# Optimization experiments

Hardware: AMD Instinct MI355X
Metric: run time of the kernel (lower is better)

## Reference

```python
import jax, jax.numpy as jnp
import numpy as np
import math

B, S, HID, H = 2, 2048, 1024, 16
D = HID // H  # head_dim = 64

def _get_slopes(n):
    # power-of-2 branch (n=16)
    start = 2 ** (-2 ** (-(math.log2(n) - 3)))
    return np.array([start * 2 ** (-i) for i in range(n)], dtype=np.float32)

def setup_inputs() -> dict:
    key = jax.random.key(0)
    ks = jax.random.split(key, 9)
    sc = 1.0 / math.sqrt(HID)
    return {
        "x":  jax.random.normal(ks[0], (B, S, HID), dtype=jnp.float32),
        "Wq": jax.random.normal(ks[1], (HID, HID), dtype=jnp.float32) * sc,
        "bq": jnp.zeros((HID,), dtype=jnp.float32),
        "Wk": jax.random.normal(ks[2], (HID, HID), dtype=jnp.float32) * sc,
        "bk": jnp.zeros((HID,), dtype=jnp.float32),
        "Wv": jax.random.normal(ks[3], (HID, HID), dtype=jnp.float32) * sc,
        "bv": jnp.zeros((HID,), dtype=jnp.float32),
        "Wo": jax.random.normal(ks[4], (HID, HID), dtype=jnp.float32) * sc,
        "bo": jnp.zeros((HID,), dtype=jnp.float32),
        "slopes": jnp.asarray(_get_slopes(H)),
    }

def reference(x, Wq, bq, Wk, bk, Wv, bv, Wo, bo, slopes):
    b, s, hid = x.shape
    h = slopes.shape[0]
    d = hid // h
    # projections (torch Linear: y = x @ W.T + b), split heads -> [b,h,s,d]
    q = (x @ Wq.T + bq).reshape(b, s, h, d).transpose(0, 2, 1, 3)
    k = (x @ Wk.T + bk).reshape(b, s, h, d).transpose(0, 2, 1, 3)
    v = (x @ Wv.T + bv).reshape(b, s, h, d).transpose(0, 2, 1, 3)
    scores = jnp.einsum('bhqd,bhkd->bhqk', q, k) / jnp.sqrt(jnp.float32(d))
    # ALiBi bias: slope_h * (j - i), shape [h,s,s]
    pos = jnp.arange(s)
    dist = (pos[None, :] - pos[:, None]).astype(x.dtype)  # [s,s]
    scores = scores + slopes[None, :, None, None] * dist[None, None]
    attn = jax.nn.softmax(scores, axis=-1)
    ctx = jnp.einsum('bhqk,bhkd->bhqd', attn, v)
    ctx = ctx.transpose(0, 2, 1, 3).reshape(b, s, hid)
    return ctx @ Wo.T + bo
```

## Files before the change

kernel.cpp:

```cpp
#include <hip/hip_runtime.h>
#include <stdint.h>

typedef __attribute__((ext_vector_type(8))) short bf16x8;
typedef __attribute__((ext_vector_type(4))) short bf16x4;
typedef __attribute__((ext_vector_type(4))) float f32x4;
typedef unsigned short u16t;

#define DEVINL static __device__ __forceinline__

DEVINL u16t f2bf(float f) {
  union { float f; unsigned u; } v; v.f = f;
  return (u16t)((v.u + 0x7FFFu + ((v.u >> 16) & 1u)) >> 16);
}

DEVINL float exp2_fast(float x) {
  float r; asm("v_exp_f32 %0, %1" : "=v"(r) : "v"(x)); return r;
}
DEVINL unsigned cvt_pk_bf16(float a, float b) {
  unsigned r; asm("v_cvt_pk_bf16_f32 %0, %1, %2" : "=v"(r) : "v"(a), "v"(b)); return r;
}

DEVINL void gload16(const void* g, void* l) {
  __builtin_amdgcn_global_load_lds((const __attribute__((address_space(1))) void*)g,
                                   (__attribute__((address_space(3))) void*)l, 16, 0, 0);
}

__global__ __launch_bounds__(256)
void cvt5_kernel(const float* __restrict__ x, const float* __restrict__ wq,
                 const float* __restrict__ wk, const float* __restrict__ wv,
                 const float* __restrict__ wo, u16t* __restrict__ x_bf,
                 u16t* __restrict__ wqkv, u16t* __restrict__ wo_bf) {
  const int bid = blockIdx.x;
  const float* src; u16t* dst; int off;
  if (bid < 2048) { src = x; dst = x_bf; off = bid * 2048; }
  else {
    const int j = bid - 2048, sel = j >> 9;
    off = (j & 511) * 2048;
    if (sel == 0)      { src = wq; dst = wqkv; }
    else if (sel == 1) { src = wk; dst = wqkv + 1048576; }
    else if (sel == 2) { src = wv; dst = wqkv + 2097152; }
    else               { src = wo; dst = wo_bf; }
  }
  const int i = off + threadIdx.x * 8;
  float4 a = *(const float4*)(src + i);
  float4 b = *(const float4*)(src + i + 4);
  union { bf16x8 v; u16t u[8]; } o;
  o.u[0] = f2bf(a.x); o.u[1] = f2bf(a.y); o.u[2] = f2bf(a.z); o.u[3] = f2bf(a.w);
  o.u[4] = f2bf(b.x); o.u[5] = f2bf(b.y); o.u[6] = f2bf(b.z); o.u[7] = f2bf(b.w);
  *(bf16x8*)(dst + i) = o.v;
}

template <int MODE>
__global__ __launch_bounds__(256, 2)
void gemm_kernel(const u16t* __restrict__ A, const u16t* __restrict__ Bw,
                 const float* __restrict__ bias0, const float* __restrict__ bias1,
                 const float* __restrict__ bias2, void* __restrict__ outp) {
  __shared__ __attribute__((aligned(16))) u16t As[128 * 64];
  __shared__ __attribute__((aligned(16))) u16t Bs[128 * 64];
  const int tid = threadIdx.x;
  const int w = tid >> 6, l = tid & 63;
  const int wm = w >> 1, wn = w & 1;
  const int bm = blockIdx.x, bn = blockIdx.y;
  const int g = l >> 4, r16 = l & 15;
  const int srow = l >> 3, sslot = l & 7;

  f32x4 acc[4][4];
#pragma unroll
  for (int m = 0; m < 4; ++m)
#pragma unroll
    for (int n = 0; n < 4; ++n) acc[m][n] = f32x4{0.f, 0.f, 0.f, 0.f};

  const size_t arow0 = (size_t)bm * 128;
  const size_t brow0 = (size_t)bn * 128;

  for (int kt = 0; kt < 16; ++kt) {
    __syncthreads();
#pragma unroll
    for (int i = 0; i < 4; ++i) {
      const int row = (i * 4 + w) * 8 + srow;
      const int colA = kt * 64 + ((sslot ^ (row & 7)) * 8);
      gload16(A + (arow0 + row) * 1024 + colA, (char*)As + (i * 4 + w) * 1024);
      gload16(Bw + (brow0 + row) * 1024 + colA, (char*)Bs + (i * 4 + w) * 1024);
    }
    asm volatile("s_waitcnt vmcnt(0)" ::: "memory");
    __syncthreads();
#pragma unroll
    for (int kk = 0; kk < 2; ++kk) {
      bf16x8 af[4], bfr[4];
#pragma unroll
      for (int m = 0; m < 4; ++m) {
        const int rr = wm * 64 + m * 16 + r16;
        af[m] = *(const bf16x8*)((const char*)As + rr * 128 + (((kk * 4 + g) ^ (rr & 7)) * 16));
      }
#pragma unroll
      for (int n = 0; n < 4; ++n) {
        const int rr = wn * 64 + n * 16 + r16;
        bfr[n] = *(const bf16x8*)((const char*)Bs + rr * 128 + (((kk * 4 + g) ^ (rr & 7)) * 16));
      }
#pragma unroll
      for (int m = 0; m < 4; ++m)
#pragma unroll
        for (int n = 0; n < 4; ++n)
          acc[m][n] = __builtin_amdgcn_mfma_f32_16x16x32_bf16(af[m], bfr[n], acc[m][n], 0, 0, 0);
    }
  }

  if (MODE == 0) {
    const int mat = bn >> 3;
    if (mat == 2) {
      u16t* vt = (u16t*)outp + 8388608u;
#pragma unroll
      for (int n = 0; n < 4; ++n) {
        const int col = ((bn & 7) * 128) + wn * 64 + n * 16 + r16;
        const int hh = col >> 6, dd = col & 63;
        const float bv = bias2[col];
#pragma unroll
        for (int m = 0; m < 4; ++m) {
          const int row0 = bm * 128 + wm * 64 + m * 16 + g * 4;
          const int b_ = row0 >> 11, s_ = row0 & 2047;
          union { bf16x4 v; u16t u[4]; } o4;
#pragma unroll
          for (int i = 0; i < 4; ++i) o4.u[i] = f2bf(acc[m][n][i] + bv);
          *(bf16x4*)(vt + ((size_t)(b_ * 16 + hh) * 64 + dd) * 2048 + s_) = o4.v;
        }
      }
    } else {
      const float* bias = (mat == 0) ? bias0 : bias1;
      const float scale = (mat == 0) ? 0.18033688f : 1.0f;
      u16t* o = (u16t*)outp + (size_t)mat * 4194304u;
#pragma unroll
      for (int n = 0; n < 4; ++n) {
        const int col = ((bn & 7) * 128) + wn * 64 + n * 16 + r16;
        const float bv = bias[col];
#pragma unroll
        for (int m = 0; m < 4; ++m) {
          const int row = bm * 128 + wm * 64 + m * 16 + g * 4;
#pragma unroll
          for (int i = 0; i < 4; ++i)
            o[(size_t)(row + i) * 1024 + col] = f2bf((acc[m][n][i] + bv) * scale);
        }
      }
    }
  } else {
    float* o = (float*)outp;
#pragma unroll
    for (int n = 0; n < 4; ++n) {
      const int col = bn * 128 + wn * 64 + n * 16 + r16;
      const float bv = bias0[col];
#pragma unroll
      for (int m = 0; m < 4; ++m) {
        const int row = bm * 128 + wm * 64 + m * 16 + g * 4;
#pragma unroll
        for (int i = 0; i < 4; ++i)
          o[(size_t)(row + i) * 1024 + col] = acc[m][n][i] + bv;
      }
    }
  }
}

__global__ __launch_bounds__(256, 2)
void attn_kernel(const u16t* __restrict__ Qb, const u16t* __restrict__ Kb,
                 const u16t* __restrict__ Vtb, const float* __restrict__ slopes,
                 u16t* __restrict__ Ctx) {
  __shared__ __attribute__((aligned(16))) u16t Kl[2][4096];
  __shared__ __attribute__((aligned(16))) u16t Vl[2][4096];
  const int tid = threadIdx.x;
  const int w = tid >> 6, l = tid & 63;
  const int g = l >> 4, r = l & 15;
  const int qt = blockIdx.x, bh = blockIdx.y;
  const int b = bh >> 4, h = bh & 15;
  const float slope2 = slopes[h] * 1.44269504f;
  const int qpos = qt * 64 + w * 16 + r;
  const size_t base = (size_t)b * 2097152 + (size_t)h * 64;

  const u16t* qrow = Qb + base + (size_t)qpos * 1024;
  const bf16x8 qf0 = *(const bf16x8*)(qrow + g * 8);
  const bf16x8 qf1 = *(const bf16x8*)(qrow + 32 + g * 8);

  const int sig = 8 * (r >> 2) + (r & 3);
  const int toffs[4] = {0, 4, 32, 36};
  int koff[4][2], voff[4][2];
#pragma unroll
  for (int t = 0; t < 4; ++t) {
    const int row = toffs[t] + sig;
    const int mk = (row & 3) ^ ((row >> 1) & 4);
#pragma unroll
    for (int hh = 0; hh < 2; ++hh) koff[t][hh] = row * 128 + (((hh * 4 + g) ^ mk) * 16);
  }
#pragma unroll
  for (int db = 0; db < 4; ++db) {
    const int row = 16 * db + r;
#pragma unroll
    for (int hh = 0; hh < 2; ++hh) voff[db][hh] = row * 128 + (((hh * 4 + g) ^ (row & 7)) * 16);
  }

  int k_row[2], k_u[2], v_u[2];
#pragma unroll
  for (int p = 0; p < 2; ++p) {
    const int line = p * 32 + w * 8 + (l >> 3);
    k_row[p] = line;
    k_u[p] = ((l & 7) ^ ((line & 3) ^ ((line >> 1) & 4))) * 8;
    v_u[p] = ((l & 7) ^ (line & 7)) * 8;
  }

  f32x4 cv[4];
#pragma unroll
  for (int t = 0; t < 4; ++t)
#pragma unroll
    for (int i = 0; i < 4; ++i) cv[t][i] = slope2 * (float)(toffs[t] + 8 * g + i);

  const float d64 = slope2 * 64.f;
  float mj = -3.0e38f;
  f32x4 oc[4], sacc;
#pragma unroll
  for (int d = 0; d < 4; ++d) oc[d] = f32x4{0.f, 0.f, 0.f, 0.f};
  sacc = f32x4{0.f, 0.f, 0.f, 0.f};
  union { bf16x8 v; u16t u[8]; } ones;
#pragma unroll
  for (int i = 0; i < 8; ++i) ones.u[i] = 0x3F80;

  const u16t* Krow = Kb + base;
  const u16t* Vrow = Vtb + (size_t)(b * 16 + h) * 131072;

#pragma unroll
  for (int p = 0; p < 2; ++p) {
    gload16(Krow + (size_t)(31 * 64 + k_row[p]) * 1024 + k_u[p],
            (char*)Kl + p * 4096 + w * 1024);
    gload16(Vrow + (size_t)k_row[p] * 2048 + 31 * 64 + v_u[p],
            (char*)Vl + p * 4096 + w * 1024);
  }

  for (int it = 0; it < 32; ++it) {
    const int kt = 31 - it;
    const int buf = it & 1;
    __syncthreads();
    if (it) mj += d64;
    if (it + 1 < 32) {
      const int nb = buf ^ 1, nkt = kt - 1;
#pragma unroll
      for (int p = 0; p < 2; ++p) {
        gload16(Krow + (size_t)(nkt * 64 + k_row[p]) * 1024 + k_u[p],
                (char*)Kl + nb * 8192 + p * 4096 + w * 1024);
        gload16(Vrow + (size_t)k_row[p] * 2048 + nkt * 64 + v_u[p],
                (char*)Vl + nb * 8192 + p * 4096 + w * 1024);
      }
    }
    const char* KB = (const char*)Kl + buf * 8192;
    const char* VB = (const char*)Vl + buf * 8192;

    f32x4 st[4];
#pragma unroll
    for (int t = 0; t < 4; ++t) {
      st[t] = __builtin_amdgcn_mfma_f32_16x16x32_bf16(
          *(const bf16x8*)(KB + koff[t][0]), qf0, cv[t], 0, 0, 0);
      st[t] = __builtin_amdgcn_mfma_f32_16x16x32_bf16(
          *(const bf16x8*)(KB + koff[t][1]), qf1, st[t], 0, 0, 0);
    }

    float tm = fmaxf(fmaxf(st[0][0], st[0][1]), fmaxf(st[0][2], st[0][3]));
    tm = fmaxf(tm, fmaxf(fmaxf(st[1][0], st[1][1]), fmaxf(st[1][2], st[1][3])));
    tm = fmaxf(tm, fmaxf(fmaxf(st[2][0], st[2][1]), fmaxf(st[2][2], st[2][3])));
    tm = fmaxf(tm, fmaxf(fmaxf(st[3][0], st[3][1]), fmaxf(st[3][2], st[3][3])));
    if (__any(tm > mj)) {
      float tr = fmaxf(tm, __shfl_xor(tm, 16));
      tr = fmaxf(tr, __shfl_xor(tr, 32));
      const float mn = fmaxf(mj, tr);
      const float corr = exp2_fast(mj - mn);
#pragma unroll
      for (int d = 0; d < 4; ++d) {
        oc[d][0] *= corr; oc[d][1] *= corr; oc[d][2] *= corr; oc[d][3] *= corr;
      }
      sacc[0] *= corr; sacc[1] *= corr; sacc[2] *= corr; sacc[3] *= corr;
      mj = mn;
    }

    float pe[16];
#pragma unroll
    for (int t = 0; t < 4; ++t)
#pragma unroll
      for (int i = 0; i < 4; ++i) pe[t * 4 + i] = exp2_fast(st[t][i] - mj);
    union { bf16x8 v; unsigned q[4]; } pb0, pb1;
#pragma unroll
    for (int j = 0; j < 4; ++j) {
      pb0.q[j] = cvt_pk_bf16(pe[j * 2], pe[j * 2 + 1]);
      pb1.q[j] = cvt_pk_bf16(pe[8 + j * 2], pe[8 + j * 2 + 1]);
    }

#pragma unroll
    for (int db = 0; db < 4; ++db) {
      oc[db] = __builtin_amdgcn_mfma_f32_16x16x32_bf16(
          *(const bf16x8*)(VB + voff[db][0]), pb0.v, oc[db], 0, 0, 0);
      oc[db] = __builtin_amdgcn_mfma_f32_16x16x32_bf16(
          *(const bf16x8*)(VB + voff[db][1]), pb1.v, oc[db], 0, 0, 0);
    }
    sacc = __builtin_amdgcn_mfma_f32_16x16x32_bf16(ones.v, pb0.v, sacc, 0, 0, 0);
    sacc = __builtin_amdgcn_mfma_f32_16x16x32_bf16(ones.v, pb1.v, sacc, 0, 0, 0);
  }

  const float inv = 1.0f / sacc[0];
  u16t* orow = Ctx + base + (size_t)qpos * 1024;
#pragma unroll
  for (int d = 0; d < 4; ++d) {
    union { bf16x4 v; u16t u[4]; } o4;
#pragma unroll
    for (int i = 0; i < 4; ++i) o4.u[i] = f2bf(oc[d][i] * inv);
    *(bf16x4*)(orow + d * 16 + g * 4) = o4.v;
  }
}

extern "C" void kernel_launch(void* const* d_in, const int* in_sizes, int n_in,
                              void* d_out, int out_size, void* d_ws, size_t ws_size,
                              hipStream_t stream) {
  const float* x = (const float*)d_in[0];
  const float* Wq = (const float*)d_in[1];
  const float* bq = (const float*)d_in[2];
  const float* Wk = (const float*)d_in[3];
  const float* bk = (const float*)d_in[4];
  const float* Wv = (const float*)d_in[5];
  const float* bv = (const float*)d_in[6];
  const float* Wo = (const float*)d_in[7];
  const float* bo = (const float*)d_in[8];
  const float* slopes = (const float*)d_in[9];
  if (ws_size < (size_t)(48u << 20)) return;
  char* ws = (char*)d_ws;
  u16t* x_bf = (u16t*)(ws);
  u16t* wqkv = (u16t*)(ws + (8u << 20));
  u16t* wo_bf = (u16t*)(ws + (14u << 20));
  u16t* q_bf = (u16t*)(ws + (16u << 20));
  u16t* ctx_bf = (u16t*)(ws + (40u << 20));

  cvt5_kernel<<<4096, 256, 0, stream>>>(x, Wq, Wk, Wv, Wo, x_bf, wqkv, wo_bf);
  gemm_kernel<0><<<dim3(32, 24), 256, 0, stream>>>(x_bf, wqkv, bq, bk, bv, (void*)q_bf);
  attn_kernel<<<dim3(32, 32), 256, 0, stream>>>(q_bf, q_bf + 4194304, q_bf + 8388608,
                                                slopes, ctx_bf);
  gemm_kernel<1><<<dim3(32, 8), 256, 0, stream>>>(ctx_bf, wo_bf, bo, bo, bo, d_out);
}
```

Measured before the change: 121.0 us.

## Triple-buffer K/V tiles with explicit vmcnt waits and use max3 reductions

```diff
diff --git a/kernel.cpp b/kernel.cpp
--- a/kernel.cpp
+++ b/kernel.cpp
@@ -18,6 +18,9 @@
 }
 DEVINL unsigned cvt_pk_bf16(float a, float b) {
   unsigned r; asm("v_cvt_pk_bf16_f32 %0, %1, %2" : "=v"(r) : "v"(a), "v"(b)); return r;
+}
+DEVINL float max3f(float a, float b, float c) {
+  float r; asm("v_max3_f32 %0, %1, %2, %3" : "=v"(r) : "v"(a), "v"(b), "v"(c)); return r;
 }
 
 DEVINL void gload16(const void* g, void* l) {
@@ -162,8 +165,8 @@
 void attn_kernel(const u16t* __restrict__ Qb, const u16t* __restrict__ Kb,
                  const u16t* __restrict__ Vtb, const float* __restrict__ slopes,
                  u16t* __restrict__ Ctx) {
-  __shared__ __attribute__((aligned(16))) u16t Kl[2][4096];
-  __shared__ __attribute__((aligned(16))) u16t Vl[2][4096];
+  __shared__ __attribute__((aligned(16))) u16t Kl[3][4096];
+  __shared__ __attribute__((aligned(16))) u16t Vl[3][4096];
   const int tid = threadIdx.x;
   const int w = tid >> 6, l = tid & 63;
   const int g = l >> 4, r = l & 15;
@@ -176,6 +179,7 @@
   const u16t* qrow = Qb + base + (size_t)qpos * 1024;
   const bf16x8 qf0 = *(const bf16x8*)(qrow + g * 8);
   const bf16x8 qf1 = *(const bf16x8*)(qrow + 32 + g * 8);
+  asm volatile("s_waitcnt vmcnt(0)" ::: "memory");
 
   const int sig = 8 * (r >> 2) + (r & 3);
   const int toffs[4] = {0, 4, 32, 36};
@@ -222,29 +226,30 @@
   const u16t* Krow = Kb + base;
   const u16t* Vrow = Vtb + (size_t)(b * 16 + h) * 131072;
 
-#pragma unroll
-  for (int p = 0; p < 2; ++p) {
-    gload16(Krow + (size_t)(31 * 64 + k_row[p]) * 1024 + k_u[p],
-            (char*)Kl + p * 4096 + w * 1024);
-    gload16(Vrow + (size_t)k_row[p] * 2048 + 31 * 64 + v_u[p],
-            (char*)Vl + p * 4096 + w * 1024);
-  }
+#define STAGE(kt_, b_)                                                              \
+  {                                                                                 \
+    _Pragma("unroll") for (int p = 0; p < 2; ++p) {                                 \
+      gload16(Krow + (size_t)((kt_) * 64 + k_row[p]) * 1024 + k_u[p],               \
+              (char*)Kl + (b_) * 8192 + p * 4096 + w * 1024);                       \
+      gload16(Vrow + (size_t)k_row[p] * 2048 + (kt_) * 64 + v_u[p],                 \
+              (char*)Vl + (b_) * 8192 + p * 4096 + w * 1024);                       \
+    }                                                                               \
+  }
+
+  STAGE(31, 0)
+  STAGE(30, 1)
 
   for (int it = 0; it < 32; ++it) {
     const int kt = 31 - it;
-    const int buf = it & 1;
-    __syncthreads();
+    const int buf = it % 3;
+    if (it == 31) { asm volatile("s_waitcnt vmcnt(0)" ::: "memory"); }
+    else          { asm volatile("s_waitcnt vmcnt(4)" ::: "memory"); }
+    __builtin_amdgcn_s_barrier();
+    asm volatile("" ::: "memory");
+    __builtin_amdgcn_sched_barrier(0);
+    if (it + 2 < 32) STAGE(kt - 2, (it + 2) % 3)
     if (it) mj += d64;
-    if (it + 1 < 32) {
-      const int nb = buf ^ 1, nkt = kt - 1;
-#pragma unroll
-      for (int p = 0; p < 2; ++p) {
-        gload16(Krow + (size_t)(nkt * 64 + k_row[p]) * 1024 + k_u[p],
-                (char*)Kl + nb * 8192 + p * 4096 + w * 1024);
-        gload16(Vrow + (size_t)k_row[p] * 2048 + nkt * 64 + v_u[p],
-                (char*)Vl + nb * 8192 + p * 4096 + w * 1024);
-      }
-    }
+
     const char* KB = (const char*)Kl + buf * 8192;
     const char* VB = (const char*)Vl + buf * 8192;
 
@@ -257,10 +262,12 @@
           *(const bf16x8*)(KB + koff[t][1]), qf1, st[t], 0, 0, 0);
     }
 
-    float tm = fmaxf(fmaxf(st[0][0], st[0][1]), fmaxf(st[0][2], st[0][3]));
-    tm = fmaxf(tm, fmaxf(fmaxf(st[1][0], st[1][1]), fmaxf(st[1][2], st[1][3])));
-    tm = fmaxf(tm, fmaxf(fmaxf(st[2][0], st[2][1]), fmaxf(st[2][2], st[2][3])));
-    tm = fmaxf(tm, fmaxf(fmaxf(st[3][0], st[3][1]), fmaxf(st[3][2], st[3][3])));
+    const float g1 = max3f(st[0][0], st[0][1], st[0][2]);
+    const float g2 = max3f(st[0][3], st[1][0], st[1][1]);
+    const float g3 = max3f(st[1][2], st[1][3], st[2][0]);
+    const float g4 = max3f(st[2][1], st[2][2], st[2][3]);
+    const float g5 = max3f(st[3][0], st[3][1], st[3][2]);
+    const float tm = fmaxf(max3f(g1, g2, g3), max3f(g4, g5, st[3][3]));
     if (__any(tm > mj)) {
       float tr = fmaxf(tm, __shfl_xor(tm, 16));
       tr = fmaxf(tr, __shfl_xor(tr, 32));
@@ -296,6 +303,7 @@
     sacc = __builtin_amdgcn_mfma_f32_16x16x32_bf16(ones.v, pb0.v, sacc, 0, 0, 0);
     sacc = __builtin_amdgcn_mfma_f32_16x16x32_bf16(ones.v, pb1.v, sacc, 0, 0, 0);
   }
+#undef STAGE
 
   const float inv = 1.0f / sacc[0];
   u16t* orow = Ctx + base + (size_t)qpos * 1024;
```

Measured after the change: 129.6 us. +7.1%, slower.
